# Kernel optimization log

Measured on AMD Instinct MI355X. Metric: run time of the kernel, lower is better.

Reference implementation:

```python
import jax, jax.numpy as jnp
import numpy as np

B, H, W, C, NB = 3, 256, 256, 16, 4
EPS = 1e-3  # keras BatchNormalization default epsilon


def _conv(x, w, b):
    y = jax.lax.conv_general_dilated(x, w, (1, 1), 'SAME',
                                     dimension_numbers=('NHWC', 'HWIO', 'NHWC'))
    return y + b


def _bn(x, g, be, mu, v):
    # inference-mode batch norm with moving statistics
    return (x - mu) * jax.lax.rsqrt(v + EPS) * g + be


def _extract_patches(x, p, s):
    # tf.image.extract_patches(..., padding='SAME') -> (b, oh, ow, p, p, c)
    b, h, w, c = x.shape
    oh, ow = -(-h // s), -(-w // s)
    pth = max((oh - 1) * s + p - h, 0)
    ptw = max((ow - 1) * s + p - w, 0)
    xp = jnp.pad(x, ((0, 0), (pth // 2, pth - pth // 2), (ptw // 2, ptw - ptw // 2), (0, 0)))
    ri = np.arange(oh)[:, None] * s + np.arange(p)[None, :]  # (oh, p)
    ci = np.arange(ow)[:, None] * s + np.arange(p)[None, :]  # (ow, p)
    return xp[:, ri[:, None, :, None], ci[None, :, None, :], :]


def setup_inputs() -> dict:
    key = jax.random.key(0)
    ks = jax.random.split(key, 4)
    mr = jax.random.normal(ks[0], (B, H, W, C), jnp.float32)
    pet = jax.random.normal(ks[1], (B, H, W, C), jnp.float32)
    W1 = jax.random.normal(ks[2], (3, 3, C, C * NB), jnp.float32) * 0.05
    W2 = jax.random.normal(ks[3], (3, 3, C * NB, C * NB), jnp.float32) * 0.05
    z = jnp.zeros((C * NB,), jnp.float32)
    o = jnp.ones((C * NB,), jnp.float32)
    return dict(mr_features=mr, pet_features=pet,
                W1=W1, b1=z, g1=o, be1=z, mu1=z, v1=o,
                W2=W2, b2=z, g2=o, be2=z, mu2=z, v2=o,
                patch=8, stride=4)


def reference(mr_features, pet_features, W1, b1, g1, be1, mu1, v1,
              W2, b2, g2, be2, mu2, v2, patch, stride):
    px = py = int(patch)
    sx = sy = int(stride)
    bsz, h, w, c = mr_features.shape

    # ---- B_Kernel_Function_Generator ----
    x = jax.nn.relu(_bn(_conv(mr_features, W1, b1), g1, be1, mu1, v1))
    x = _bn(_conv(x, W2, b2), g2, be2, mu2, v2)  # last conv_block: no activation
    nb = x.shape[-1] // c
    x = x.reshape(bsz, h, w, c, nb)
    x = jax.nn.softmax(x, axis=-1)
    b_features = jnp.where(x > 1e-5, x, 0.0)  # mask * x

    # ---- Sparse_Kernel_Matrix_Multiplication ----
    bc, bf = c, nb
    Nx, Ny = h // px, w // py
    lx, ly = px // sx, py // sy
    SNx, SNy = Nx * lx, Ny * ly

    bflat = b_features.reshape(bsz, h, w, bc * bf)
    bp = _extract_patches(bflat, px, sx).reshape(bsz, SNx, SNy, px, py, bc, bf)
    pp = _extract_patches(pet_features, px, sx).reshape(bsz, SNx, SNy, px, py, bc, 1)

    dn = jnp.sum(bp, axis=(3, 4), keepdims=True)              # diagonal norm
    kp = jnp.sum(pp * bp, axis=(3, 4), keepdims=True)         # kernel-weighted PET
    dn_safe = jnp.where(dn == 0, 1.0, dn)
    kn = jnp.where(dn == 0, 0.0, kp / dn_safe) * bp           # divide_no_nan
    kpet = jnp.sum(kn, axis=-1)                               # (b,SNx,SNy,px,py,bc)

    # deinterleave stride phases: kernel_pet[:, i::lx, j::ly] stack
    kp6 = kpet.reshape(bsz, Nx, lx, Ny, ly, px, py, c)
    st = kp6.transpose(4, 2, 0, 1, 3, 5, 6, 7).reshape(lx * ly, bsz, Nx, Ny, px, py, c)
    t = st.transpose(1, 2, 3, 4, 5, 6, 0).reshape(bsz, Nx, Ny, px, py, c, lx, ly)
    t = t.transpose(0, 1, 3, 2, 4, 5, 6, 7).reshape(bsz, Nx * px, Ny * py, c, lx, ly)
    t = t.transpose(4, 5, 0, 1, 2, 3)  # (lx, ly, b, H, W, c)

    # align_patches: roll each shifted copy back into registration, then mean
    rev = t.transpose(2, 3, 4, 5, 0, 1).reshape(bsz, h, w, c, lx * ly)
    rev = rev.transpose(4, 0, 1, 2, 3)  # (lx*ly, b, H, W, c)
    rollx = np.arange(-px // 2 + sx // 2, px // 2 + sx // 2, sx)
    rolly = np.arange(-py // 2 + sy // 2, py // 2 + sy // 2, sy)
    acc = jnp.zeros((bsz, h, w, c), rev.dtype)
    for m in range(lx * ly):  # small fixed set (lx*ly = 4)
        acc = acc + jnp.roll(rev[m], (int(rollx[m % lx]), int(rolly[m // lx])), axis=(1, 2))
    return acc / (lx * ly)
```

## Files before the change

### kernel.cpp

```cpp
#include <hip/hip_runtime.h>

#define EPSB 1e-3f

typedef _Float16 half8 __attribute__((ext_vector_type(8)));
typedef _Float16 half4 __attribute__((ext_vector_type(4)));
typedef float f32x4 __attribute__((ext_vector_type(4)));

__global__ __launch_bounds__(256, 4)
void k_prep(const float* __restrict__ W1, const float* __restrict__ W2,
            const float* __restrict__ b1, const float* __restrict__ g1,
            const float* __restrict__ be1, const float* __restrict__ mu1,
            const float* __restrict__ v1,
            const float* __restrict__ b2, const float* __restrict__ g2,
            const float* __restrict__ be2, const float* __restrict__ mu2,
            const float* __restrict__ v2,
            _Float16* __restrict__ W1F, _Float16* __restrict__ W2F,
            float* __restrict__ ST)
{
    int t = blockIdx.x * 256 + threadIdx.x;
    if (t < 5 * 4 * 64 * 8) {
        int k = t & 7, lane = (t >> 3) & 63, snt = t >> 9;
        int s = snt >> 2, ct = snt & 3;
        int quad = lane >> 4, n16 = lane & 15;
        int tap = 2 * s + (quad >> 1);
        int ci  = (quad & 1) * 8 + k;
        int co  = ct * 16 + n16;
        float v = (tap < 9) ? W1[(tap * 16 + ci) * 64 + co] : 0.f;
        W1F[t] = (_Float16)v;
        return;
    }
    t -= 5 * 4 * 64 * 8;
    if (t < 18 * 4 * 64 * 8) {
        int k = t & 7, lane = (t >> 3) & 63, snt = t >> 9;
        int s = snt >> 2, ct = snt & 3;
        int quad = lane >> 4, n16 = lane & 15;
        int tap = s >> 1;
        int ci  = (s & 1) * 32 + quad * 8 + k;
        int co  = ct * 16 + n16;
        W2F[t] = (_Float16)W2[(tap * 64 + ci) * 64 + co];
        return;
    }
    t -= 18 * 4 * 64 * 8;
    if (t < 256) {
        int c = t & 63, sel = t >> 6;
        if (sel == 0)      ST[c]       = g1[c] * rsqrtf(v1[c] + EPSB);
        else if (sel == 1) ST[64 + c]  = (b1[c] - mu1[c]) * (g1[c] * rsqrtf(v1[c] + EPSB)) + be1[c];
        else if (sel == 2) ST[128 + c] = g2[c] * rsqrtf(v2[c] + EPSB);
        else               ST[192 + c] = (b2[c] - mu2[c]) * (g2[c] * rsqrtf(v2[c] + EPSB)) + be2[c];
    }
}

#define CIP1 24
__global__ __launch_bounds__(256, 3)
void k_conv1(const float* __restrict__ mr, const _Float16* __restrict__ W1F,
             const float* __restrict__ ST, _Float16* __restrict__ A)
{
    __shared__ __align__(16) _Float16 sM[4 * 64 * 72];
    const int tid = threadIdx.x;
    const int b  = blockIdx.y;
    const int r0 = (blockIdx.x >> 2) * 4;
    const int q0 = (blockIdx.x & 3) * 64;

    for (int idx = tid; idx < 6 * 66 * 2; idx += 256) {
        int c = idx & 1, pp = idx >> 1;
        int p = pp % 66, dy = pp / 66;
        int rr = r0 + dy - 1, qg = q0 + p - 1;
        half8 h = (half8)(_Float16)0.f;
        if ((unsigned)rr < 256u && (unsigned)qg < 256u) {
            const float* src = mr + ((b * 256 + rr) * 256 + qg) * 16 + c * 8;
            float4 v0 = *(const float4*)src;
            float4 v1 = *(const float4*)(src + 4);
            h = (half8){(_Float16)v0.x, (_Float16)v0.y, (_Float16)v0.z, (_Float16)v0.w,
                        (_Float16)v1.x, (_Float16)v1.y, (_Float16)v1.z, (_Float16)v1.w};
        }
        *(half8*)(&sM[(dy * 66 + p) * CIP1 + c * 8]) = h;
    }
    __syncthreads();

    const int w = tid >> 6, lane = tid & 63;
    const int n16 = lane & 15, quad = lane >> 4;
    const int ci0 = (quad & 1) * 8;

    f32x4 acc[4][4];
    #pragma unroll
    for (int i = 0; i < 4; ++i)
        #pragma unroll
        for (int j = 0; j < 4; ++j) acc[i][j] = (f32x4){0.f, 0.f, 0.f, 0.f};

    #pragma unroll
    for (int s = 0; s < 5; ++s) {
        int tap  = 2 * s + (quad >> 1);
        int tapc = tap > 8 ? 8 : tap;
        int dy = tapc / 3, dx = tapc % 3;
        half8 wfrag[4], pfrag[4];
        #pragma unroll
        for (int ct = 0; ct < 4; ++ct)
            wfrag[ct] = *(const half8*)(W1F + ((s * 4 + ct) * 64 + lane) * 8);
        #pragma unroll
        for (int qt = 0; qt < 4; ++qt)
            pfrag[qt] = *(const half8*)&sM[((w + dy) * 66 + qt * 16 + n16 + dx) * CIP1 + ci0];
        #pragma unroll
        for (int qt = 0; qt < 4; ++qt)
            #pragma unroll
            for (int ct = 0; ct < 4; ++ct)
                acc[qt][ct] = __builtin_amdgcn_mfma_f32_16x16x32_f16(wfrag[ct], pfrag[qt], acc[qt][ct], 0, 0, 0);
    }

    half4 hv[4][4];
    #pragma unroll
    for (int ct = 0; ct < 4; ++ct) {
        int co0 = ct * 16 + quad * 4;
        f32x4 sc = *(const f32x4*)&ST[co0];
        f32x4 sh = *(const f32x4*)&ST[64 + co0];
        #pragma unroll
        for (int qt = 0; qt < 4; ++qt) {
            half4 h;
            #pragma unroll
            for (int j = 0; j < 4; ++j)
                h[j] = (_Float16)fmaxf(acc[qt][ct][j] * sc[j] + sh[j], 0.f);
            hv[ct][qt] = h;
        }
    }
    __syncthreads();
    #pragma unroll
    for (int ct = 0; ct < 4; ++ct) {
        int co0 = ct * 16 + quad * 4;
        #pragma unroll
        for (int qt = 0; qt < 4; ++qt) {
            int ql = qt * 16 + n16;
            *(half4*)(&sM[(w * 64 + ql) * 72 + co0]) = hv[ct][qt];
        }
    }
    __syncthreads();

    for (int idx = tid; idx < 2048; idx += 256) {
        int rl2 = idx >> 9, rest = idx & 511;
        int ql = rest >> 3, seg = rest & 7;
        int4 v = *(const int4*)&sM[(rl2 * 64 + ql) * 72 + seg * 8];
        *(int4*)(A + (((b * 256 + r0 + rl2) * 256 + q0 + ql) * 64 + seg * 8)) = v;
    }
}

#define CIP2 72
__global__ __launch_bounds__(256, 2)
void k_conv2(const _Float16* __restrict__ A, const _Float16* __restrict__ W2F,
             const float* __restrict__ ST, const float* __restrict__ pet,
             _Float16* __restrict__ BF, float* __restrict__ S2)
{
    __shared__ __align__(16) _Float16 sM[6 * 66 * CIP2];
    const int tid = threadIdx.x;
    const int b  = blockIdx.y;
    const int r0 = (blockIdx.x >> 2) * 4;
    const int q0 = (blockIdx.x & 3) * 64;

    for (int idx = tid; idx < 6 * 66 * 8; idx += 256) {
        int c = idx & 7, pp = idx >> 3;
        int p = pp % 66, dy = pp / 66;
        int rr = r0 + dy - 1, qg = q0 + p - 1;
        int4 v = {0, 0, 0, 0};
        if ((unsigned)rr < 256u && (unsigned)qg < 256u)
            v = *(const int4*)(A + (((b * 256 + rr) * 256 + qg) * 64 + c * 8));
        *(int4*)(&sM[(dy * 66 + p) * CIP2 + c * 8]) = v;
    }
    __syncthreads();

    const int w = tid >> 6, lane = tid & 63;
    const int n16 = lane & 15, quad = lane >> 4;

    f32x4 acc[4][4];
    #pragma unroll
    for (int i = 0; i < 4; ++i)
        #pragma unroll
        for (int j = 0; j < 4; ++j) acc[i][j] = (f32x4){0.f, 0.f, 0.f, 0.f};

    #pragma unroll
    for (int s = 0; s < 18; ++s) {
        const int tap = s >> 1;
        const int dy = tap / 3, dx = tap % 3;
        const int ci0 = (s & 1) * 32 + quad * 8;
        half8 wfrag[4], pfrag[4];
        #pragma unroll
        for (int ct = 0; ct < 4; ++ct)
            wfrag[ct] = *(const half8*)(W2F + ((s * 4 + ct) * 64 + lane) * 8);
        #pragma unroll
        for (int qt = 0; qt < 4; ++qt)
            pfrag[qt] = *(const half8*)&sM[((w + dy) * 66 + qt * 16 + n16 + dx) * CIP2 + ci0];
        #pragma unroll
        for (int qt = 0; qt < 4; ++qt)
            #pragma unroll
            for (int ct = 0; ct < 4; ++ct)
                acc[qt][ct] = __builtin_amdgcn_mfma_f32_16x16x32_f16(wfrag[ct], pfrag[qt], acc[qt][ct], 0, 0, 0);
    }

    half4 hv[4][4];
    #pragma unroll
    for (int ct = 0; ct < 4; ++ct) {
        int co0 = ct * 16 + quad * 4;
        f32x4 sc = *(const f32x4*)&ST[128 + co0];
        f32x4 sh = *(const f32x4*)&ST[192 + co0];
        #pragma unroll
        for (int qt = 0; qt < 4; ++qt) {
            float z0 = acc[qt][ct][0] * sc[0] + sh[0];
            float z1 = acc[qt][ct][1] * sc[1] + sh[1];
            float z2 = acc[qt][ct][2] * sc[2] + sh[2];
            float z3 = acc[qt][ct][3] * sc[3] + sh[3];
            float mx = fmaxf(fmaxf(z0, z1), fmaxf(z2, z3));
            float e0 = __expf(z0 - mx), e1 = __expf(z1 - mx);
            float e2 = __expf(z2 - mx), e3 = __expf(z3 - mx);
            float inv = __builtin_amdgcn_rcpf((e0 + e1) + (e2 + e3));
            float p0 = e0 * inv, p1 = e1 * inv, p2 = e2 * inv, p3 = e3 * inv;
            half4 h;
            h[0] = (_Float16)(p0 > 1e-5f ? p0 : 0.f);
            h[1] = (_Float16)(p1 > 1e-5f ? p1 : 0.f);
            h[2] = (_Float16)(p2 > 1e-5f ? p2 : 0.f);
            h[3] = (_Float16)(p3 > 1e-5f ? p3 : 0.f);
            hv[ct][qt] = h;
        }
    }
    __syncthreads();
    #pragma unroll
    for (int ct = 0; ct < 4; ++ct) {
        int co0 = ct * 16 + quad * 4;
        #pragma unroll
        for (int qt = 0; qt < 4; ++qt) {
            int ql = qt * 16 + n16;
            *(half4*)(&sM[(w * 64 + ql) * CIP2 + co0]) = hv[ct][qt];
        }
    }
    __syncthreads();

    for (int idx = tid; idx < 2048; idx += 256) {
        int rl2 = idx >> 9, rest = idx & 511;
        int ql = rest >> 3, seg = rest & 7;
        int4 v = *(const int4*)&sM[(rl2 * 64 + ql) * CIP2 + seg * 8];
        *(int4*)(BF + (((b * 256 + r0 + rl2) * 256 + q0 + ql) * 64 + seg * 8)) = v;
    }

    const int qp = tid >> 3, chg = tid & 7;
    #pragma unroll
    for (int cr = 0; cr < 2; ++cr) {
        float dn[8], kp[8];
        #pragma unroll
        for (int j = 0; j < 8; ++j) { dn[j] = 0.f; kp[j] = 0.f; }
        #pragma unroll
        for (int u = 0; u < 2; ++u)
            #pragma unroll
            for (int v = 0; v < 2; ++v) {
                int rl = 2 * cr + u, ql = 2 * qp + v;
                half8 bf = *(const half8*)(&sM[(rl * 64 + ql) * CIP2 + chg * 8]);
                float2 p2 = *(const float2*)(pet + ((b * 256 + r0 + rl) * 256 + q0 + ql) * 16 + chg * 2);
                #pragma unroll
                for (int j = 0; j < 8; ++j) {
                    float bv = (float)bf[j];
                    dn[j] += bv;
                    kp[j] = fmaf((j < 4) ? p2.x : p2.y, bv, kp[j]);
                }
            }
        float* o = S2 + 2 * ((size_t)(((b * 128 + (r0 >> 1) + cr) * 128 + (q0 >> 1) + qp) * 64) + chg * 8);
        #pragma unroll
        for (int m = 0; m < 4; ++m)
            *(float4*)(o + 4 * m) = make_float4(dn[2*m], kp[2*m], dn[2*m+1], kp[2*m+1]);
    }
}

__global__ __launch_bounds__(256, 4)
void k_ratio(const float* __restrict__ S2, float* __restrict__ RATIO)
{
    int t = blockIdx.x * 256 + threadIdx.x;
    int cf = t & 63;
    int j  = (t >> 6) & 63;
    int i  = (t >> 12) & 63;
    int b  = t >> 18;
    float dn = 0.f, kp = 0.f;
    #pragma unroll
    for (int u = 0; u < 4; ++u) {
        int r2 = 2 * i - 1 + u;
        if ((unsigned)r2 >= 128u) continue;
        #pragma unroll
        for (int v = 0; v < 4; ++v) {
            int q2 = 2 * j - 1 + v;
            if ((unsigned)q2 >= 128u) continue;
            float2 s = *(const float2*)(S2 + 2 * (((b * 128 + r2) * 128 + q2) * 64 + cf));
            dn += s.x;
            kp += s.y;
        }
    }
    RATIO[t] = (dn == 0.f) ? 0.f : 0.25f * kp * __builtin_amdgcn_rcpf(dn);
}

__global__ __launch_bounds__(256, 4)
void k_out(const _Float16* __restrict__ BF, const float* __restrict__ RATIO,
           float* __restrict__ out)
{
    __shared__ __align__(16) float sU[64 * 68];
    const int tid = threadIdx.x;
    const int r = blockIdx.x & 255;
    const int b = blockIdx.x >> 8;

    const int i0 = (r <= 253) ? 2 * ((r + 2) >> 3)       : -1;
    const int i1 = (r >= 2)   ? 2 * ((r - 2) >> 3) + 1   : -1;

    for (int idx = tid; idx < 1024; idx += 256) {
        int j = idx >> 4, c4 = idx & 15;
        float4 a = make_float4(0.f, 0.f, 0.f, 0.f);
        if (i0 >= 0) a = *(const float4*)&RATIO[(((b * 64 + i0) * 64 + j) << 6) + 4 * c4];
        float4 bb = make_float4(0.f, 0.f, 0.f, 0.f);
        if (i1 >= 0) bb = *(const float4*)&RATIO[(((b * 64 + i1) * 64 + j) << 6) + 4 * c4];
        *(float4*)&sU[j * 68 + 4 * c4] = make_float4(a.x + bb.x, a.y + bb.y, a.z + bb.z, a.w + bb.w);
    }
    __syncthreads();

    const int q = tid;
    const int j0 = (q <= 253) ? 2 * ((q + 2) >> 3)     : -1;
    const int j1 = (q >= 2)   ? 2 * ((q - 2) >> 3) + 1 : -1;

    const half8* bfp = (const half8*)(BF + ((size_t)(b * 256 + r) * 256 + q) * 64);
    float o[16];
    #pragma unroll
    for (int c = 0; c < 16; ++c) o[c] = 0.f;

    #pragma unroll
    for (int c2 = 0; c2 < 8; ++c2) {
        half8 bf8 = bfp[c2];
        float s0 = 0.f, s1 = 0.f;
        #pragma unroll
        for (int pj = 0; pj < 2; ++pj) {
            int jj = pj ? j1 : j0;
            if (jj < 0) continue;
            const float* up = &sU[jj * 68 + 8 * c2];
            s0 += (float)bf8[0] * up[0] + (float)bf8[1] * up[1]
                + (float)bf8[2] * up[2] + (float)bf8[3] * up[3];
            s1 += (float)bf8[4] * up[4] + (float)bf8[5] * up[5]
                + (float)bf8[6] * up[6] + (float)bf8[7] * up[7];
        }
        o[2 * c2]     = s0;
        o[2 * c2 + 1] = s1;
    }
    float* op = out + ((size_t)(b * 256 + r) * 256 + q) * 16;
    #pragma unroll
    for (int m = 0; m < 4; ++m)
        *(float4*)(op + 4 * m) = make_float4(o[4*m], o[4*m+1], o[4*m+2], o[4*m+3]);
}

extern "C" void kernel_launch(void* const* d_in, const int* in_sizes, int n_in,
                              void* d_out, int out_size, void* d_ws, size_t ws_size,
                              hipStream_t stream) {
    const float* mr  = (const float*)d_in[0];
    const float* pet = (const float*)d_in[1];
    const float* W1  = (const float*)d_in[2];
    const float* b1  = (const float*)d_in[3];
    const float* g1  = (const float*)d_in[4];
    const float* be1 = (const float*)d_in[5];
    const float* mu1 = (const float*)d_in[6];
    const float* v1  = (const float*)d_in[7];
    const float* W2  = (const float*)d_in[8];
    const float* b2  = (const float*)d_in[9];
    const float* g2  = (const float*)d_in[10];
    const float* be2 = (const float*)d_in[11];
    const float* mu2 = (const float*)d_in[12];
    const float* v2  = (const float*)d_in[13];

    char* ws = (char*)d_ws;
    _Float16* A     = (_Float16*)(ws);
    _Float16* BF    = (_Float16*)(ws + 25165824);
    float*    S2    = (float*)(ws + 50331648);
    float*    RATIO = (float*)(ws + 75497472);
    _Float16* W1F   = (_Float16*)(ws + 78643200);
    _Float16* W2F   = (_Float16*)(ws + 78663680);
    float*    ST    = (float*)(ws + 78737408);
    float*    out   = (float*)d_out;

    dim3 blk(256);
    k_prep<<<185, blk, 0, stream>>>(W1, W2, b1, g1, be1, mu1, v1,
                                    b2, g2, be2, mu2, v2, W1F, W2F, ST);
    k_conv1<<<dim3(256, 3), blk, 0, stream>>>(mr, W1F, ST, A);
    k_conv2<<<dim3(256, 3), blk, 0, stream>>>(A, W2F, ST, pet, BF, S2);
    k_ratio<<<3072, blk, 0, stream>>>(S2, RATIO);
    k_out<<<768, blk, 0, stream>>>(BF, RATIO, out);
}
```

Measured before the change: 173.2 us.

## Fuse conv1 into conv2 with halo recompute and store S2 in half precision

```diff
diff --git a/kernel.cpp b/kernel.cpp
--- a/kernel.cpp
+++ b/kernel.cpp
@@ -4,6 +4,7 @@
 
 typedef _Float16 half8 __attribute__((ext_vector_type(8)));
 typedef _Float16 half4 __attribute__((ext_vector_type(4)));
+typedef _Float16 half2v __attribute__((ext_vector_type(2)));
 typedef float f32x4 __attribute__((ext_vector_type(4)));
 
 __global__ __launch_bounds__(256, 4)
@@ -51,20 +52,23 @@
 }
 
 #define CIP1 24
-__global__ __launch_bounds__(256, 3)
-void k_conv1(const float* __restrict__ mr, const _Float16* __restrict__ W1F,
-             const float* __restrict__ ST, _Float16* __restrict__ A)
+#define CIP2 72
+__global__ __launch_bounds__(256, 2)
+void k_conv(const float* __restrict__ mr, const _Float16* __restrict__ W1F,
+            const _Float16* __restrict__ W2F, const float* __restrict__ ST,
+            const float* __restrict__ pet,
+            _Float16* __restrict__ BF, _Float16* __restrict__ S2h)
 {
-    __shared__ __align__(16) _Float16 sM[4 * 64 * 72];
+    __shared__ __align__(16) _Float16 sM[6 * 66 * CIP2];
     const int tid = threadIdx.x;
     const int b  = blockIdx.y;
     const int r0 = (blockIdx.x >> 2) * 4;
     const int q0 = (blockIdx.x & 3) * 64;
 
-    for (int idx = tid; idx < 6 * 66 * 2; idx += 256) {
+    for (int idx = tid; idx < 8 * 68 * 2; idx += 256) {
         int c = idx & 1, pp = idx >> 1;
-        int p = pp % 66, dy = pp / 66;
-        int rr = r0 + dy - 1, qg = q0 + p - 1;
+        int p = pp % 68, dy = pp / 68;
+        int rr = r0 + dy - 2, qg = q0 + p - 2;
         half8 h = (half8)(_Float16)0.f;
         if ((unsigned)rr < 256u && (unsigned)qg < 256u) {
             const float* src = mr + ((b * 256 + rr) * 256 + qg) * 16 + c * 8;
@@ -73,99 +77,70 @@
             h = (half8){(_Float16)v0.x, (_Float16)v0.y, (_Float16)v0.z, (_Float16)v0.w,
                         (_Float16)v1.x, (_Float16)v1.y, (_Float16)v1.z, (_Float16)v1.w};
         }
-        *(half8*)(&sM[(dy * 66 + p) * CIP1 + c * 8]) = h;
+        *(half8*)(&sM[(dy * 72 + p) * CIP1 + c * 8]) = h;
     }
     __syncthreads();
 
     const int w = tid >> 6, lane = tid & 63;
     const int n16 = lane & 15, quad = lane >> 4;
-    const int ci0 = (quad & 1) * 8;
-
-    f32x4 acc[4][4];
-    #pragma unroll
-    for (int i = 0; i < 4; ++i)
-        #pragma unroll
-        for (int j = 0; j < 4; ++j) acc[i][j] = (f32x4){0.f, 0.f, 0.f, 0.f};
-
-    #pragma unroll
-    for (int s = 0; s < 5; ++s) {
-        int tap  = 2 * s + (quad >> 1);
-        int tapc = tap > 8 ? 8 : tap;
-        int dy = tapc / 3, dx = tapc % 3;
-        half8 wfrag[4], pfrag[4];
-        #pragma unroll
-        for (int ct = 0; ct < 4; ++ct)
-            wfrag[ct] = *(const half8*)(W1F + ((s * 4 + ct) * 64 + lane) * 8);
-        #pragma unroll
-        for (int qt = 0; qt < 4; ++qt)
-            pfrag[qt] = *(const half8*)&sM[((w + dy) * 66 + qt * 16 + n16 + dx) * CIP1 + ci0];
-        #pragma unroll
-        for (int qt = 0; qt < 4; ++qt)
-            #pragma unroll
-            for (int ct = 0; ct < 4; ++ct)
-                acc[qt][ct] = __builtin_amdgcn_mfma_f32_16x16x32_f16(wfrag[ct], pfrag[qt], acc[qt][ct], 0, 0, 0);
-    }
-
-    half4 hv[4][4];
-    #pragma unroll
-    for (int ct = 0; ct < 4; ++ct) {
-        int co0 = ct * 16 + quad * 4;
-        f32x4 sc = *(const f32x4*)&ST[co0];
-        f32x4 sh = *(const f32x4*)&ST[64 + co0];
-        #pragma unroll
-        for (int qt = 0; qt < 4; ++qt) {
-            half4 h;
-            #pragma unroll
-            for (int j = 0; j < 4; ++j)
-                h[j] = (_Float16)fmaxf(acc[qt][ct][j] * sc[j] + sh[j], 0.f);
-            hv[ct][qt] = h;
-        }
-    }
-    __syncthreads();
-    #pragma unroll
-    for (int ct = 0; ct < 4; ++ct) {
-        int co0 = ct * 16 + quad * 4;
-        #pragma unroll
-        for (int qt = 0; qt < 4; ++qt) {
-            int ql = qt * 16 + n16;
-            *(half4*)(&sM[(w * 64 + ql) * 72 + co0]) = hv[ct][qt];
-        }
-    }
-    __syncthreads();
-
-    for (int idx = tid; idx < 2048; idx += 256) {
-        int rl2 = idx >> 9, rest = idx & 511;
-        int ql = rest >> 3, seg = rest & 7;
-        int4 v = *(const int4*)&sM[(rl2 * 64 + ql) * 72 + seg * 8];
-        *(int4*)(A + (((b * 256 + r0 + rl2) * 256 + q0 + ql) * 64 + seg * 8)) = v;
-    }
-}
-
-#define CIP2 72
-__global__ __launch_bounds__(256, 2)
-void k_conv2(const _Float16* __restrict__ A, const _Float16* __restrict__ W2F,
-             const float* __restrict__ ST, const float* __restrict__ pet,
-             _Float16* __restrict__ BF, float* __restrict__ S2)
-{
-    __shared__ __align__(16) _Float16 sM[6 * 66 * CIP2];
-    const int tid = threadIdx.x;
-    const int b  = blockIdx.y;
-    const int r0 = (blockIdx.x >> 2) * 4;
-    const int q0 = (blockIdx.x & 3) * 64;
-
-    for (int idx = tid; idx < 6 * 66 * 8; idx += 256) {
-        int c = idx & 7, pp = idx >> 3;
-        int p = pp % 66, dy = pp / 66;
-        int rr = r0 + dy - 1, qg = q0 + p - 1;
-        int4 v = {0, 0, 0, 0};
-        if ((unsigned)rr < 256u && (unsigned)qg < 256u)
-            v = *(const int4*)(A + (((b * 256 + rr) * 256 + qg) * 64 + c * 8));
-        *(int4*)(&sM[(dy * 66 + p) * CIP2 + c * 8]) = v;
-    }
-    __syncthreads();
-
-    const int w = tid >> 6, lane = tid & 63;
-    const int n16 = lane & 15, quad = lane >> 4;
+    const _Float16* W1l = W1F + lane * 8;
+    const _Float16* W2l = W2F + lane * 8;
+
+    half4 hv1[8][4];
+    #pragma unroll
+    for (int k = 0; k < 8; ++k) {
+        int u = w * 8 + k;
+        if (u < 30) {
+            int row = u / 5, qt = u - 5 * row;
+            f32x4 a1[4];
+            #pragma unroll
+            for (int ct = 0; ct < 4; ++ct) a1[ct] = (f32x4){0.f, 0.f, 0.f, 0.f};
+            #pragma unroll
+            for (int s = 0; s < 5; ++s) {
+                int tap  = 2 * s + (quad >> 1);
+                int tapc = tap > 8 ? 8 : tap;
+                int dy = tapc / 3, dx = tapc % 3;
+                int mc = qt * 16 + n16 + dx;
+                mc = mc > 67 ? 67 : mc;
+                half8 pf = *(const half8*)&sM[((row + dy) * 72 + mc) * CIP1 + (quad & 1) * 8];
+                #pragma unroll
+                for (int ct = 0; ct < 4; ++ct) {
+                    half8 wf = *(const half8*)(W1l + (s * 4 + ct) * 512);
+                    a1[ct] = __builtin_amdgcn_mfma_f32_16x16x32_f16(wf, pf, a1[ct], 0, 0, 0);
+                }
+            }
+            #pragma unroll
+            for (int ct = 0; ct < 4; ++ct) {
+                int co0 = ct * 16 + quad * 4;
+                f32x4 sc = *(const f32x4*)&ST[co0];
+                f32x4 sh = *(const f32x4*)&ST[64 + co0];
+                half4 h;
+                #pragma unroll
+                for (int j = 0; j < 4; ++j)
+                    h[j] = (_Float16)fmaxf(a1[ct][j] * sc[j] + sh[j], 0.f);
+                hv1[k][ct] = h;
+            }
+        }
+    }
+    __syncthreads();
+
+    #pragma unroll
+    for (int k = 0; k < 8; ++k) {
+        int u = w * 8 + k;
+        if (u < 30) {
+            int row = u / 5, qt = u - 5 * row;
+            int ac = qt * 16 + n16;
+            if (ac < 66) {
+                bool in = ((unsigned)(r0 - 1 + row) < 256u) && ((unsigned)(q0 - 1 + ac) < 256u);
+                #pragma unroll
+                for (int ct = 0; ct < 4; ++ct) {
+                    half4 h = in ? hv1[k][ct] : (half4)(_Float16)0.f;
+                    *(half4*)(&sM[(row * 66 + ac) * CIP2 + ct * 16 + quad * 4]) = h;
+                }
+            }
+        }
+    }
+    __syncthreads();
 
     f32x4 acc[4][4];
     #pragma unroll
@@ -181,7 +156,7 @@
         half8 wfrag[4], pfrag[4];
         #pragma unroll
         for (int ct = 0; ct < 4; ++ct)
-            wfrag[ct] = *(const half8*)(W2F + ((s * 4 + ct) * 64 + lane) * 8);
+            wfrag[ct] = *(const half8*)(W2l + (s * 4 + ct) * 512);
         #pragma unroll
         for (int qt = 0; qt < 4; ++qt)
             pfrag[qt] = *(const half8*)&sM[((w + dy) * 66 + qt * 16 + n16 + dx) * CIP2 + ci0];
@@ -256,15 +231,22 @@
                     kp[j] = fmaf((j < 4) ? p2.x : p2.y, bv, kp[j]);
                 }
             }
-        float* o = S2 + 2 * ((size_t)(((b * 128 + (r0 >> 1) + cr) * 128 + (q0 >> 1) + qp) * 64) + chg * 8);
-        #pragma unroll
-        for (int m = 0; m < 4; ++m)
-            *(float4*)(o + 4 * m) = make_float4(dn[2*m], kp[2*m], dn[2*m+1], kp[2*m+1]);
+        _Float16* o = S2h + 2 * ((size_t)(((b * 128 + (r0 >> 1) + cr) * 128 + (q0 >> 1) + qp) * 64) + chg * 8);
+        #pragma unroll
+        for (int m = 0; m < 2; ++m) {
+            half8 h;
+            #pragma unroll
+            for (int j = 0; j < 4; ++j) {
+                h[2 * j]     = (_Float16)dn[4 * m + j];
+                h[2 * j + 1] = (_Float16)kp[4 * m + j];
+            }
+            *(half8*)(o + 8 * m) = h;
+        }
     }
 }
 
 __global__ __launch_bounds__(256, 4)
-void k_ratio(const float* __restrict__ S2, float* __restrict__ RATIO)
+void k_ratio(const _Float16* __restrict__ S2h, float* __restrict__ RATIO)
 {
     int t = blockIdx.x * 256 + threadIdx.x;
     int cf = t & 63;
@@ -280,9 +262,9 @@
         for (int v = 0; v < 4; ++v) {
             int q2 = 2 * j - 1 + v;
             if ((unsigned)q2 >= 128u) continue;
-            float2 s = *(const float2*)(S2 + 2 * (((b * 128 + r2) * 128 + q2) * 64 + cf));
-            dn += s.x;
-            kp += s.y;
+            half2v s = *(const half2v*)(S2h + 2 * (((b * 128 + r2) * 128 + q2) * 64 + cf));
+            dn += (float)s[0];
+            kp += (float)s[1];
         }
     }
     RATIO[t] = (dn == 0.f) ? 0.f : 0.25f * kp * __builtin_amdgcn_rcpf(dn);
@@ -361,20 +343,18 @@
     const float* v2  = (const float*)d_in[13];
 
     char* ws = (char*)d_ws;
-    _Float16* A     = (_Float16*)(ws);
-    _Float16* BF    = (_Float16*)(ws + 25165824);
-    float*    S2    = (float*)(ws + 50331648);
-    float*    RATIO = (float*)(ws + 75497472);
-    _Float16* W1F   = (_Float16*)(ws + 78643200);
-    _Float16* W2F   = (_Float16*)(ws + 78663680);
-    float*    ST    = (float*)(ws + 78737408);
+    _Float16* BF    = (_Float16*)(ws);
+    _Float16* S2h   = (_Float16*)(ws + 25165824);
+    float*    RATIO = (float*)(ws + 37748736);
+    _Float16* W1F   = (_Float16*)(ws + 40894464);
+    _Float16* W2F   = (_Float16*)(ws + 40914944);
+    float*    ST    = (float*)(ws + 40988672);
     float*    out   = (float*)d_out;
 
     dim3 blk(256);
     k_prep<<<185, blk, 0, stream>>>(W1, W2, b1, g1, be1, mu1, v1,
                                     b2, g2, be2, mu2, v2, W1F, W2F, ST);
-    k_conv1<<<dim3(256, 3), blk, 0, stream>>>(mr, W1F, ST, A);
-    k_conv2<<<dim3(256, 3), blk, 0, stream>>>(A, W2F, ST, pet, BF, S2);
-    k_ratio<<<3072, blk, 0, stream>>>(S2, RATIO);
+    k_conv<<<dim3(256, 3), blk, 0, stream>>>(mr, W1F, W2F, ST, pet, BF, S2h);
+    k_ratio<<<3072, blk, 0, stream>>>(S2h, RATIO);
     k_out<<<768, blk, 0, stream>>>(BF, RATIO, out);
 }
```

Measured after the change: 171.4 us. No clear change (-1.0%).

## Read conv operands straight from padded global buffer and store partial sums in fp16

Applied to the files above, without the earlier changes.

```diff
diff --git a/kernel.cpp b/kernel.cpp
--- a/kernel.cpp
+++ b/kernel.cpp
@@ -4,6 +4,7 @@
 
 typedef _Float16 half8 __attribute__((ext_vector_type(8)));
 typedef _Float16 half4 __attribute__((ext_vector_type(4)));
+typedef _Float16 half2v __attribute__((ext_vector_type(2)));
 typedef float f32x4 __attribute__((ext_vector_type(4)));
 
 __global__ __launch_bounds__(256, 4)
@@ -50,7 +51,23 @@
     }
 }
 
-#define CIP1 24
+__global__ __launch_bounds__(256, 4)
+void k_zero(_Float16* __restrict__ A)
+{
+    int t = blockIdx.x * 256 + threadIdx.x;
+    if (t >= 3 * 1028 * 8) return;
+    int b = t / 8224;
+    int rem = t - b * 8224;
+    int px = rem >> 3, seg = rem & 7;
+    int row, col;
+    if (px < 258)      { row = 0;        col = px; }
+    else if (px < 516) { row = 257;      col = px - 258; }
+    else if (px < 772) { row = px - 515; col = 0; }
+    else               { row = px - 771; col = 257; }
+    int4 z = {0, 0, 0, 0};
+    *(int4*)(A + (((size_t)b * 258 + row) * 258 + col) * 64 + seg * 8) = z;
+}
+
 __global__ __launch_bounds__(256, 3)
 void k_conv1(const float* __restrict__ mr, const _Float16* __restrict__ W1F,
              const float* __restrict__ ST, _Float16* __restrict__ A)
@@ -60,26 +77,10 @@
     const int b  = blockIdx.y;
     const int r0 = (blockIdx.x >> 2) * 4;
     const int q0 = (blockIdx.x & 3) * 64;
-
-    for (int idx = tid; idx < 6 * 66 * 2; idx += 256) {
-        int c = idx & 1, pp = idx >> 1;
-        int p = pp % 66, dy = pp / 66;
-        int rr = r0 + dy - 1, qg = q0 + p - 1;
-        half8 h = (half8)(_Float16)0.f;
-        if ((unsigned)rr < 256u && (unsigned)qg < 256u) {
-            const float* src = mr + ((b * 256 + rr) * 256 + qg) * 16 + c * 8;
-            float4 v0 = *(const float4*)src;
-            float4 v1 = *(const float4*)(src + 4);
-            h = (half8){(_Float16)v0.x, (_Float16)v0.y, (_Float16)v0.z, (_Float16)v0.w,
-                        (_Float16)v1.x, (_Float16)v1.y, (_Float16)v1.z, (_Float16)v1.w};
-        }
-        *(half8*)(&sM[(dy * 66 + p) * CIP1 + c * 8]) = h;
-    }
-    __syncthreads();
-
     const int w = tid >> 6, lane = tid & 63;
     const int n16 = lane & 15, quad = lane >> 4;
-    const int ci0 = (quad & 1) * 8;
+    const int r = r0 + w;
+    const _Float16* W1l = W1F + lane * 8;
 
     f32x4 acc[4][4];
     #pragma unroll
@@ -89,24 +90,32 @@
 
     #pragma unroll
     for (int s = 0; s < 5; ++s) {
+        half8 wf[4];
+        #pragma unroll
+        for (int ct = 0; ct < 4; ++ct)
+            wf[ct] = *(const half8*)(W1l + (s * 4 + ct) * 512);
         int tap  = 2 * s + (quad >> 1);
         int tapc = tap > 8 ? 8 : tap;
         int dy = tapc / 3, dx = tapc % 3;
-        half8 wfrag[4], pfrag[4];
-        #pragma unroll
-        for (int ct = 0; ct < 4; ++ct)
-            wfrag[ct] = *(const half8*)(W1F + ((s * 4 + ct) * 64 + lane) * 8);
-        #pragma unroll
-        for (int qt = 0; qt < 4; ++qt)
-            pfrag[qt] = *(const half8*)&sM[((w + dy) * 66 + qt * 16 + n16 + dx) * CIP1 + ci0];
-        #pragma unroll
-        for (int qt = 0; qt < 4; ++qt)
+        int rr = r + dy - 1;
+        bool rok = (unsigned)rr < 256u;
+        #pragma unroll
+        for (int qt = 0; qt < 4; ++qt) {
+            int qg = q0 + qt * 16 + n16 + dx - 1;
+            bool ok = rok && ((unsigned)qg < 256u);
+            const float* src = mr + (((b * 256 + (ok ? rr : 0)) * 256 + (ok ? qg : 0)) * 16
+                                     + (quad & 1) * 8);
+            float4 v0 = *(const float4*)src;
+            float4 v1 = *(const float4*)(src + 4);
+            half8 pf = ok ? (half8){(_Float16)v0.x, (_Float16)v0.y, (_Float16)v0.z, (_Float16)v0.w,
+                                    (_Float16)v1.x, (_Float16)v1.y, (_Float16)v1.z, (_Float16)v1.w}
+                          : (half8)(_Float16)0.f;
             #pragma unroll
             for (int ct = 0; ct < 4; ++ct)
-                acc[qt][ct] = __builtin_amdgcn_mfma_f32_16x16x32_f16(wfrag[ct], pfrag[qt], acc[qt][ct], 0, 0, 0);
-    }
-
-    half4 hv[4][4];
+                acc[qt][ct] = __builtin_amdgcn_mfma_f32_16x16x32_f16(wf[ct], pf, acc[qt][ct], 0, 0, 0);
+        }
+    }
+
     #pragma unroll
     for (int ct = 0; ct < 4; ++ct) {
         int co0 = ct * 16 + quad * 4;
@@ -118,54 +127,41 @@
             #pragma unroll
             for (int j = 0; j < 4; ++j)
                 h[j] = (_Float16)fmaxf(acc[qt][ct][j] * sc[j] + sh[j], 0.f);
-            hv[ct][qt] = h;
+            *(half4*)(&sM[w * 4608 + (qt * 16 + n16) * 72 + co0]) = h;
         }
     }
     __syncthreads();
-    #pragma unroll
-    for (int ct = 0; ct < 4; ++ct) {
-        int co0 = ct * 16 + quad * 4;
-        #pragma unroll
-        for (int qt = 0; qt < 4; ++qt) {
-            int ql = qt * 16 + n16;
-            *(half4*)(&sM[(w * 64 + ql) * 72 + co0]) = hv[ct][qt];
-        }
-    }
-    __syncthreads();
 
     for (int idx = tid; idx < 2048; idx += 256) {
-        int rl2 = idx >> 9, rest = idx & 511;
+        int rl = idx >> 9, rest = idx & 511;
         int ql = rest >> 3, seg = rest & 7;
-        int4 v = *(const int4*)&sM[(rl2 * 64 + ql) * 72 + seg * 8];
-        *(int4*)(A + (((b * 256 + r0 + rl2) * 256 + q0 + ql) * 64 + seg * 8)) = v;
-    }
-}
-
-#define CIP2 72
-__global__ __launch_bounds__(256, 2)
+        int4 v = *(const int4*)&sM[rl * 4608 + ql * 72 + seg * 8];
+        *(int4*)(A + (((size_t)b * 258 + (r0 + rl + 1)) * 258 + (q0 + ql + 1)) * 64 + seg * 8) = v;
+    }
+}
+
+__global__ __launch_bounds__(256, 3)
 void k_conv2(const _Float16* __restrict__ A, const _Float16* __restrict__ W2F,
              const float* __restrict__ ST, const float* __restrict__ pet,
-             _Float16* __restrict__ BF, float* __restrict__ S2)
-{
-    __shared__ __align__(16) _Float16 sM[6 * 66 * CIP2];
+             _Float16* __restrict__ BF, _Float16* __restrict__ S2h)
+{
+    __shared__ __align__(16) _Float16 sM[4 * 64 * 72];
     const int tid = threadIdx.x;
     const int b  = blockIdx.y;
     const int r0 = (blockIdx.x >> 2) * 4;
     const int q0 = (blockIdx.x & 3) * 64;
-
-    for (int idx = tid; idx < 6 * 66 * 8; idx += 256) {
-        int c = idx & 7, pp = idx >> 3;
-        int p = pp % 66, dy = pp / 66;
-        int rr = r0 + dy - 1, qg = q0 + p - 1;
-        int4 v = {0, 0, 0, 0};
-        if ((unsigned)rr < 256u && (unsigned)qg < 256u)
-            v = *(const int4*)(A + (((b * 256 + rr) * 256 + qg) * 64 + c * 8));
-        *(int4*)(&sM[(dy * 66 + p) * CIP2 + c * 8]) = v;
-    }
-    __syncthreads();
-
     const int w = tid >> 6, lane = tid & 63;
     const int n16 = lane & 15, quad = lane >> 4;
+    const int r = r0 + w;
+    const _Float16* W2l = W2F + lane * 8;
+
+    const _Float16* pb[3][4];
+    #pragma unroll
+    for (int dy = 0; dy < 3; ++dy)
+        #pragma unroll
+        for (int qt = 0; qt < 4; ++qt)
+            pb[dy][qt] = A + (((size_t)b * 258 + r + dy) * 258 + (q0 + qt * 16 + n16)) * 64
+                           + quad * 8;
 
     f32x4 acc[4][4];
     #pragma unroll
@@ -177,22 +173,21 @@
     for (int s = 0; s < 18; ++s) {
         const int tap = s >> 1;
         const int dy = tap / 3, dx = tap % 3;
-        const int ci0 = (s & 1) * 32 + quad * 8;
-        half8 wfrag[4], pfrag[4];
+        const int cio = (s & 1) * 32;
+        half8 wf[4], pf[4];
         #pragma unroll
         for (int ct = 0; ct < 4; ++ct)
-            wfrag[ct] = *(const half8*)(W2F + ((s * 4 + ct) * 64 + lane) * 8);
+            wf[ct] = *(const half8*)(W2l + (s * 4 + ct) * 512);
         #pragma unroll
         for (int qt = 0; qt < 4; ++qt)
-            pfrag[qt] = *(const half8*)&sM[((w + dy) * 66 + qt * 16 + n16 + dx) * CIP2 + ci0];
+            pf[qt] = *(const half8*)(pb[dy][qt] + dx * 64 + cio);
         #pragma unroll
         for (int qt = 0; qt < 4; ++qt)
             #pragma unroll
             for (int ct = 0; ct < 4; ++ct)
-                acc[qt][ct] = __builtin_amdgcn_mfma_f32_16x16x32_f16(wfrag[ct], pfrag[qt], acc[qt][ct], 0, 0, 0);
-    }
-
-    half4 hv[4][4];
+                acc[qt][ct] = __builtin_amdgcn_mfma_f32_16x16x32_f16(wf[ct], pf[qt], acc[qt][ct], 0, 0, 0);
+    }
+
     #pragma unroll
     for (int ct = 0; ct < 4; ++ct) {
         int co0 = ct * 16 + quad * 4;
@@ -214,26 +209,16 @@
             h[1] = (_Float16)(p1 > 1e-5f ? p1 : 0.f);
             h[2] = (_Float16)(p2 > 1e-5f ? p2 : 0.f);
             h[3] = (_Float16)(p3 > 1e-5f ? p3 : 0.f);
-            hv[ct][qt] = h;
+            *(half4*)(&sM[w * 4608 + (qt * 16 + n16) * 72 + co0]) = h;
         }
     }
     __syncthreads();
-    #pragma unroll
-    for (int ct = 0; ct < 4; ++ct) {
-        int co0 = ct * 16 + quad * 4;
-        #pragma unroll
-        for (int qt = 0; qt < 4; ++qt) {
-            int ql = qt * 16 + n16;
-            *(half4*)(&sM[(w * 64 + ql) * CIP2 + co0]) = hv[ct][qt];
-        }
-    }
-    __syncthreads();
 
     for (int idx = tid; idx < 2048; idx += 256) {
-        int rl2 = idx >> 9, rest = idx & 511;
+        int rl = idx >> 9, rest = idx & 511;
         int ql = rest >> 3, seg = rest & 7;
-        int4 v = *(const int4*)&sM[(rl2 * 64 + ql) * CIP2 + seg * 8];
-        *(int4*)(BF + (((b * 256 + r0 + rl2) * 256 + q0 + ql) * 64 + seg * 8)) = v;
+        int4 v = *(const int4*)&sM[rl * 4608 + ql * 72 + seg * 8];
+        *(int4*)(BF + (((b * 256 + r0 + rl) * 256 + q0 + ql) * 64 + seg * 8)) = v;
     }
 
     const int qp = tid >> 3, chg = tid & 7;
@@ -247,7 +232,7 @@
             #pragma unroll
             for (int v = 0; v < 2; ++v) {
                 int rl = 2 * cr + u, ql = 2 * qp + v;
-                half8 bf = *(const half8*)(&sM[(rl * 64 + ql) * CIP2 + chg * 8]);
+                half8 bf = *(const half8*)(&sM[rl * 4608 + ql * 72 + chg * 8]);
                 float2 p2 = *(const float2*)(pet + ((b * 256 + r0 + rl) * 256 + q0 + ql) * 16 + chg * 2);
                 #pragma unroll
                 for (int j = 0; j < 8; ++j) {
@@ -256,15 +241,22 @@
                     kp[j] = fmaf((j < 4) ? p2.x : p2.y, bv, kp[j]);
                 }
             }
-        float* o = S2 + 2 * ((size_t)(((b * 128 + (r0 >> 1) + cr) * 128 + (q0 >> 1) + qp) * 64) + chg * 8);
-        #pragma unroll
-        for (int m = 0; m < 4; ++m)
-            *(float4*)(o + 4 * m) = make_float4(dn[2*m], kp[2*m], dn[2*m+1], kp[2*m+1]);
+        _Float16* o = S2h + 2 * ((size_t)(((b * 128 + (r0 >> 1) + cr) * 128 + (q0 >> 1) + qp) * 64) + chg * 8);
+        #pragma unroll
+        for (int m = 0; m < 2; ++m) {
+            half8 h;
+            #pragma unroll
+            for (int j = 0; j < 4; ++j) {
+                h[2 * j]     = (_Float16)dn[4 * m + j];
+                h[2 * j + 1] = (_Float16)kp[4 * m + j];
+            }
+            *(half8*)(o + 8 * m) = h;
+        }
     }
 }
 
 __global__ __launch_bounds__(256, 4)
-void k_ratio(const float* __restrict__ S2, float* __restrict__ RATIO)
+void k_ratio(const _Float16* __restrict__ S2h, float* __restrict__ RATIO)
 {
     int t = blockIdx.x * 256 + threadIdx.x;
     int cf = t & 63;
@@ -280,9 +272,9 @@
         for (int v = 0; v < 4; ++v) {
             int q2 = 2 * j - 1 + v;
             if ((unsigned)q2 >= 128u) continue;
-            float2 s = *(const float2*)(S2 + 2 * (((b * 128 + r2) * 128 + q2) * 64 + cf));
-            dn += s.x;
-            kp += s.y;
+            half2v s = *(const half2v*)(S2h + 2 * (((b * 128 + r2) * 128 + q2) * 64 + cf));
+            dn += (float)s[0];
+            kp += (float)s[1];
         }
     }
     RATIO[t] = (dn == 0.f) ? 0.f : 0.25f * kp * __builtin_amdgcn_rcpf(dn);
@@ -362,19 +354,20 @@
 
     char* ws = (char*)d_ws;
     _Float16* A     = (_Float16*)(ws);
-    _Float16* BF    = (_Float16*)(ws + 25165824);
-    float*    S2    = (float*)(ws + 50331648);
-    float*    RATIO = (float*)(ws + 75497472);
-    _Float16* W1F   = (_Float16*)(ws + 78643200);
-    _Float16* W2F   = (_Float16*)(ws + 78663680);
-    float*    ST    = (float*)(ws + 78737408);
+    _Float16* BF    = (_Float16*)(ws + 25560576);
+    _Float16* S2h   = (_Float16*)(ws + 50726400);
+    float*    RATIO = (float*)(ws + 63309312);
+    _Float16* W1F   = (_Float16*)(ws + 66455040);
+    _Float16* W2F   = (_Float16*)(ws + 66475520);
+    float*    ST    = (float*)(ws + 66549248);
     float*    out   = (float*)d_out;
 
     dim3 blk(256);
     k_prep<<<185, blk, 0, stream>>>(W1, W2, b1, g1, be1, mu1, v1,
                                     b2, g2, be2, mu2, v2, W1F, W2F, ST);
+    k_zero<<<97, blk, 0, stream>>>(A);
     k_conv1<<<dim3(256, 3), blk, 0, stream>>>(mr, W1F, ST, A);
-    k_conv2<<<dim3(256, 3), blk, 0, stream>>>(A, W2F, ST, pet, BF, S2);
-    k_ratio<<<3072, blk, 0, stream>>>(S2, RATIO);
+    k_conv2<<<dim3(256, 3), blk, 0, stream>>>(A, W2F, ST, pet, BF, S2h);
+    k_ratio<<<3072, blk, 0, stream>>>(S2h, RATIO);
     k_out<<<768, blk, 0, stream>>>(BF, RATIO, out);
 }
```

Measured after the change: 178.2 us. 1.03x slower.
